# Kernel tuning notes

Hardware: AMD Instinct MI355X
Metric: run time of the kernel (lower is better)

## Reference

```python
import jax, jax.numpy as jnp
import numpy as np

N_NODES = 100000
K_NEIGH = 32
N_SAMPLE = 32
ITEM_LO, ITEM_HI = 0, 49999
EPS = 1e-12


def setup_inputs():
    key = jax.random.key(0)
    ks = jax.random.split(key, 16)
    B, T = 2048, 50
    D0, H, D2 = 64, 32, 64
    NU = 20000

    def nrm(k, shape, scale=0.05):
        return jax.random.normal(k, shape, dtype=jnp.float32) * scale

    return {
        "users": jax.random.randint(ks[0], (B,), 0, NU, dtype=jnp.int32),
        "pos": jax.random.randint(ks[1], (B,), 0, ITEM_HI + 1, dtype=jnp.int32),
        "neg": jax.random.randint(ks[2], (B,), 0, ITEM_HI + 1, dtype=jnp.int32),
        "train_set": jax.random.randint(ks[3], (B, T), 0, ITEM_HI + 1, dtype=jnp.int32),
        "adj_matrix": jax.random.randint(ks[4], (N_NODES, K_NEIGH), 0, N_NODES, dtype=jnp.int32),
        "edge_matrix": jax.random.randint(ks[5], (N_NODES, K_NEIGH), 0, N_NODES, dtype=jnp.int32),
        "entity_embedding": nrm(ks[6], (N_NODES, D0)),
        "Wl1": nrm(ks[7], (H, D0), 0.1),
        "bl1": jnp.zeros((H,), jnp.float32),
        "Wr1": nrm(ks[8], (H, D0), 0.1),
        "Wl2": nrm(ks[9], (D2, H), 0.1),
        "bl2": jnp.zeros((D2,), jnp.float32),
        "Wr2": nrm(ks[10], (D2, H), 0.1),
        "dis_user": nrm(ks[11], (NU, D2)),
        "dis_item": nrm(ks[12], (N_NODES, D2)),
    }


def _dropout(x, k, p=0.5):
    keep = jax.random.bernoulli(k, 1.0 - p, x.shape)
    return jnp.where(keep, x / (1.0 - p), 0.0)


def reference(users, pos, neg, train_set, adj_matrix, edge_matrix,
              entity_embedding, Wl1, bl1, Wr1, Wl2, bl2, Wr2,
              dis_user, dis_item):
    B = users.shape[0]
    # edge list: src = node_index repeated, dst = its sampled neighbors (build_edge)
    src = jnp.repeat(jnp.arange(N_NODES, dtype=jnp.int32), K_NEIGH)
    dst = edge_matrix.reshape(-1)
    cnt = jax.ops.segment_sum(jnp.ones_like(dst, jnp.float32), dst, num_segments=N_NODES)
    inv_cnt = (1.0 / jnp.maximum(cnt, 1.0))[:, None]

    def sage(x, Wl, bl, Wr):
        # PyG SAGEConv: lin_l(mean of messages at dst) + lin_r(x)
        agg = jax.ops.segment_sum(x[src], dst, num_segments=N_NODES) * inv_cnt
        return agg @ Wl.T + bl + x @ Wr.T

    def gcn(call_id):
        k = jax.random.fold_in(jax.random.key(42), call_id)
        k1, k2 = jax.random.split(k)
        h = _dropout(jax.nn.leaky_relu(sage(entity_embedding, Wl1, bl1, Wr1), 0.01), k1)
        h = _dropout(sage(h, Wl2, bl2, Wr2), k2)
        return h / jnp.maximum(jnp.linalg.norm(h, axis=1, keepdims=True), EPS)

    def kg_step(pos_ids, call_id, step):
        g = gcn(call_id)
        u_e = g[users]                    # [B,d]
        pos_e = g[pos_ids]                # [B,d]
        one_hop = adj_matrix[pos_ids]     # [B,K]
        i_e = g[one_hop]                  # [B,K,d]
        p = jnp.einsum('bkd,bd->bk', i_e, pos_e * u_e)
        logp = jax.nn.log_softmax(p, axis=1)
        if step == 1:
            nid = jnp.argmax(p, axis=1)[:, None]
        else:
            # torch.sort is ascending -> first num_sample are the LOWEST logits (as in source)
            nid = jnp.argsort(p, axis=1)[:, :N_SAMPLE]
        cand = jnp.take_along_axis(one_hop, nid, axis=1)
        clog = jnp.take_along_axis(logp, nid, axis=1)
        if step == 1:
            return cand[:, 0], clog[:, 0]
        return cand, clog

    def filter_entity(cand, k):
        rnd = jax.random.randint(k, cand.shape, ITEM_LO, ITEM_HI + 1, dtype=cand.dtype)
        bad = (cand < ITEM_LO) | (cand > ITEM_HI)
        return jnp.where(bad, rnd, cand)

    def dis_step(cand, clog):
        ranking = jnp.einsum('bd,bnd->bn', dis_user[users], dis_item[cand])
        idx = jnp.argmax(ranking, axis=1)[:, None]
        return (jnp.take_along_axis(cand, idx, axis=1)[:, 0],
                jnp.take_along_axis(clog, idx, axis=1)[:, 0])

    def filter_trainset(gneg):
        in_tr = jnp.any(gneg[:, None] == train_set, axis=1)
        return jnp.where(in_tr, neg, gneg)

    def one_round(pos_ids, base):
        oh, l1 = kg_step(pos_ids, base, 1)
        cand, l2 = kg_step(oh, base + 1, 2)
        cand = filter_entity(cand, jax.random.fold_in(jax.random.key(7), base))
        gneg, lsel = dis_step(cand, l2)
        gneg = filter_trainset(gneg)
        return gneg, l1 + lsel

    g1, lg1 = one_round(pos, 0)
    g2, lg2 = one_round(g1, 2)
    good_neg = jnp.stack([g1, g2], axis=1)        # [B, k_step]
    good_logits = jnp.stack([lg1, lg2], axis=1)   # [B, k_step]
    return good_neg, good_logits
```

## Files before the change

kernel.cpp:

```cpp
#include <hip/hip_runtime.h>
#include <hip/hip_bf16.h>
#include <stdint.h>

#define NND 100000
#define KN 32
#define NE (NND*KN)
#define BB 2048
#define TT 50
#define DD0 64
#define HH 32
#define DD2 64
#define NROWS 34
#define BSH 9
#define NBUK ((NND + (1<<BSH) - 1) >> BSH)
#define PCHUNK 6250

typedef unsigned long long ull;

__device__ __forceinline__ void tf2x32(uint32_t k0, uint32_t k1, uint32_t& x0, uint32_t& x1){
  uint32_t k2 = k0 ^ k1 ^ 0x1BD11BDAu;
#define TFR(r) { x0 += x1; x1 = (x1<<(r)) | (x1>>(32-(r))); x1 ^= x0; }
  x0 += k0; x1 += k1;
  TFR(13) TFR(15) TFR(26) TFR(6)
  x0 += k1; x1 += k2 + 1u;
  TFR(17) TFR(29) TFR(16) TFR(24)
  x0 += k2; x1 += k0 + 2u;
  TFR(13) TFR(15) TFR(26) TFR(6)
  x0 += k0; x1 += k1 + 3u;
  TFR(17) TFR(29) TFR(16) TFR(24)
  x0 += k1; x1 += k2 + 4u;
  TFR(13) TFR(15) TFR(26) TFR(6)
  x0 += k2; x1 += k0 + 5u;
#undef TFR
}

__device__ __forceinline__ uint32_t xorbits(uint32_t ka, uint32_t kb, uint32_t i){
  uint32_t x0=0u, x1=i;
  tf2x32(ka,kb,x0,x1);
  return x0^x1;
}

__global__ void keys_kernel(uint32_t* keys, int* bcnt){
  int t=threadIdx.x;
  for(int i=t;i<NBUK+1;i+=64) bcnt[i]=0;
  if(t==0 && blockIdx.x==0){
    for(int cid=0;cid<4;++cid){
      uint32_t K0=0u,K1=(uint32_t)cid;
      tf2x32(0u,42u,K0,K1);
      uint32_t a0=0u,a1=0u; tf2x32(K0,K1,a0,a1);
      uint32_t b0=0u,b1=1u; tf2x32(K0,K1,b0,b1);
      keys[cid*4+0]=a0; keys[cid*4+1]=a1;
      keys[cid*4+2]=b0; keys[cid*4+3]=b1;
    }
    for(int r=0;r<2;++r){
      uint32_t F0=0u,F1=(uint32_t)(2*r);
      tf2x32(0u,7u,F0,F1);
      uint32_t a0=0u,a1=0u; tf2x32(F0,F1,a0,a1);
      uint32_t b0=0u,b1=1u; tf2x32(F0,F1,b0,b1);
      keys[16+r*4+0]=a0; keys[16+r*4+1]=a1;
      keys[16+r*4+2]=b0; keys[16+r*4+3]=b1;
    }
  }
}

__global__ void __launch_bounds__(256) bcount_kernel(const int* __restrict__ edge, int* bcnt){
  __shared__ int h[NBUK];
  int t=threadIdx.x;
  for(int i=t;i<NBUK;i+=256) h[i]=0;
  __syncthreads();
  int start=blockIdx.x*PCHUNK, end=start+PCHUNK;
  for(int e=start+t;e<end;e+=256) atomicAdd(&h[edge[e]>>BSH],1);
  __syncthreads();
  for(int i=t;i<NBUK;i+=256) if(h[i]) atomicAdd(&bcnt[i],h[i]);
}

__global__ void bscan_kernel(const int* bcnt, int* boff, int* bcur, int* off){
  if(threadIdx.x==0 && blockIdx.x==0){
    int run=0;
    for(int i=0;i<NBUK;++i){ boff[i]=run; bcur[i]=run; run+=bcnt[i]; }
    boff[NBUK]=run;
    off[NND]=NE;
  }
}

__global__ void __launch_bounds__(256) bscatter_kernel(const int* __restrict__ edge,
    int* bcur, ull* __restrict__ tmp8){
  __shared__ int h[NBUK], base[NBUK], lcur[NBUK];
  int t=threadIdx.x;
  for(int i=t;i<NBUK;i+=256){ h[i]=0; lcur[i]=0; }
  __syncthreads();
  int start=blockIdx.x*PCHUNK, end=start+PCHUNK;
  for(int e=start+t;e<end;e+=256) atomicAdd(&h[edge[e]>>BSH],1);
  __syncthreads();
  for(int i=t;i<NBUK;i+=256) base[i] = h[i]? atomicAdd(&bcur[i],h[i]) : 0;
  __syncthreads();
  for(int e=start+t;e<end;e+=256){
    int d=edge[e];
    int b=d>>BSH;
    int r=atomicAdd(&lcur[b],1);
    tmp8[base[b]+r] = (((ull)(unsigned)d)<<32) | (unsigned)e;
  }
}

__global__ void __launch_bounds__(256) bucket_csr_kernel(const int* __restrict__ boff,
    const ull* __restrict__ tmp8, int* __restrict__ off, float* __restrict__ inv,
    int* __restrict__ col){
  __shared__ int cnt[512], pref[512], cur2[512];
  int b=blockIdx.x, t=threadIdx.x;
  int nb=b<<BSH;
  for(int i=t;i<512;i+=256) cnt[i]=0;
  __syncthreads();
  int lo=boff[b], hi=boff[b+1];
  for(int i=lo+t;i<hi;i+=256){
    int ld=(int)(tmp8[i]>>32)-nb;
    atomicAdd(&cnt[ld],1);
  }
  __syncthreads();
  if(t==0){ int run=lo; for(int i=0;i<512;++i){ pref[i]=run; cur2[i]=run; run+=cnt[i]; } }
  __syncthreads();
  for(int i=t;i<512;i+=256){
    int d=nb+i;
    if(d<NND){ off[d]=pref[i]; int c=cnt[i]; inv[d]=1.0f/(float)(c>0?c:1); }
  }
  __syncthreads();
  for(int i=lo+t;i<hi;i+=256){
    ull v=tmp8[i];
    int ld=(int)(v>>32)-nb;
    int r=atomicAdd(&cur2[ld],1);
    col[r]=(int)(v&0xffffffffu);
  }
}

__global__ void count_kernel(const int* dst, int* cnt){
  int e = blockIdx.x*256 + threadIdx.x;
  if(e < NE) atomicAdd(&cnt[dst[e]], 1);
}
__global__ void scan_kernel(const int* cnt, int* off, int* cur, float* inv){
  __shared__ int part[1024];
  int t = threadIdx.x;
  const int CH = (NND + 1023)/1024;
  int lo = t*CH, hi = lo+CH; if(hi>NND) hi=NND;
  int s=0;
  for(int i=lo;i<hi;++i) s += cnt[i];
  part[t]=s;
  __syncthreads();
  if(t==0){ int run=0; for(int i=0;i<1024;++i){ int v=part[i]; part[i]=run; run+=v; } }
  __syncthreads();
  int run = part[t];
  for(int i=lo;i<hi;++i){
    off[i]=run; cur[i]=run;
    int c=cnt[i];
    inv[i]=1.0f/(float)(c>0?c:1);
    run+=c;
  }
  if(t==0) off[NND]=NE;
}
__global__ void fill_kernel(const int* dst, int* cur, int* col){
  int e = blockIdx.x*256 + threadIdx.x;
  if(e < NE){
    int d = dst[e];
    int slot = atomicAdd(&cur[d],1);
    col[slot] = e;
  }
}

__global__ void __launch_bounds__(256) sortseg_wave_kernel(const int* off, int* col){
  int t=threadIdx.x, lane=t&63, w=t>>6;
  int node = blockIdx.x*4 + w;
  if(node>=NND) return;
  int lo=off[node], hi=off[node+1];
  int deg=hi-lo;
  if(deg<=1) return;
  if(deg<=64){
    int v = (lane<deg)? col[lo+lane] : 0x7fffffff;
    for(int p=0;p<64;++p){
      int partner;
      if((p&1)==0) partner = lane^1;
      else partner = (lane==0||lane==63)? lane : ((lane&1)? lane+1 : lane-1);
      int pv = __shfl(v, partner, 64);
      if(partner>lane) v = v<pv? v:pv;
      else if(partner<lane) v = v>pv? v:pv;
    }
    if(lane<deg) col[lo+lane]=v;
  } else if(lane==0){
    for(int i=lo+1;i<hi;++i){
      int v=col[i]; int j=i-1;
      while(j>=lo && col[j]>v){ col[j+1]=col[j]; --j; }
      col[j+1]=v;
    }
  }
}

__device__ __forceinline__ float gather_seq(const float* __restrict__ src, int S, int d,
    const int* __restrict__ col, int lo, int hi, int lane){
  float acc=0.f;
  int deg=hi-lo, base=0;
  while(base<deg){
    int rem=deg-base; int cw = rem<64?rem:64;
    int cv = col[lo+base+ (lane<cw?lane:cw-1)];
    for(int k=0;k<cw;k+=16){
      int m=cw-k;
      float v[16];
#pragma unroll
      for(int j=0;j<16;++j){
        int q = (j<m)? k+j : k;
        int s = __shfl(cv,q,64)>>5;
        v[j] = src[(size_t)s*S+d];
      }
#pragma unroll
      for(int j=0;j<16;++j) if(j<m) acc += v[j];
    }
    base+=cw;
  }
  return acc;
}

__device__ __forceinline__ float gather_seq32(const float* __restrict__ src, int S, int d,
    const int* __restrict__ col, int lo, int hi, int l){
  float acc=0.f;
  int deg=hi-lo, base=0;
  while(base<deg){
    int rem=deg-base; int cw = rem<32?rem:32;
    int cv = col[lo+base+ (l<cw?l:cw-1)];
    for(int k=0;k<cw;k+=16){
      int m=cw-k;
      float v[16];
#pragma unroll
      for(int j=0;j<16;++j){
        int q = (j<m)? k+j : k;
        int s = __shfl(cv,q,32)>>5;
        v[j] = src[(size_t)s*S+d];
      }
#pragma unroll
      for(int j=0;j<16;++j) if(j<m) acc += v[j];
    }
    base+=cw;
  }
  return acc;
}

__global__ void __launch_bounds__(512) sage1base_kernel(const float* __restrict__ x,
    const int* __restrict__ off, const int* __restrict__ col,
    const float* __restrict__ inv, const float* __restrict__ Wl,
    const float* __restrict__ bl, const float* __restrict__ Wr,
    float* __restrict__ h1base){
  __shared__ float sWlT[DD0*HH], sWrT[DD0*HH];
  __shared__ float sA[8][DD0], sX[8][DD0];
  int t=threadIdx.x, lane=t&63, w=t>>6;
  for(int j=t;j<HH*DD0;j+=512){
    int k=j>>5, h=j&31;
    sWlT[j]=Wl[h*DD0+k]; sWrT[j]=Wr[h*DD0+k];
  }
  int node=blockIdx.x*8+w;
  int lo=off[node], hi=off[node+1];
  float acc=gather_seq(x,DD0,lane,col,lo,hi,lane);
  acc *= inv[node];
  sA[w][lane]=acc;
  sX[w][lane]=x[(size_t)node*DD0+lane];
  __syncthreads();
  if(lane<HH){
    float s1=0.f, s2=0.f;
    for(int k=0;k<DD0;++k){
      s1 += sA[w][k]*sWlT[k*HH+lane];
      s2 += sX[w][k]*sWrT[k*HH+lane];
    }
    float v=s1+bl[lane]+s2;
    v = (v>=0.f) ? v : 0.01f*v;
    h1base[(size_t)node*HH+lane]=v;
  }
}

__global__ void __launch_bounds__(256) mask_kernel(const float* __restrict__ h1base,
    const uint32_t* __restrict__ keys, int cid, float* __restrict__ h1){
  int j = blockIdx.x*256 + threadIdx.x;
  if(j < NND*HH){
    uint32_t bits = xorbits(keys[cid*4+0],keys[cid*4+1],(uint32_t)j);
    float v = h1base[j];
    h1[j] = ((bits>>31)==0u) ? 2.f*v : 0.f;
  }
}

__global__ void __launch_bounds__(256) sage1_kernel(const float* __restrict__ x,
    const int* __restrict__ off, const int* __restrict__ col,
    const float* __restrict__ inv, const float* __restrict__ Wl,
    const float* __restrict__ bl, const float* __restrict__ Wr,
    const uint32_t* __restrict__ keys, int cid, float* __restrict__ h1o){
  __shared__ float sWlT[DD0*HH], sWrT[DD0*HH];
  __shared__ float sA[4][DD0], sX[4][DD0];
  int t=threadIdx.x, lane=t&63, w=t>>6;
  for(int j=t;j<HH*DD0;j+=256){
    int k=j>>5, h=j&31;
    sWlT[j]=Wl[h*DD0+k]; sWrT[j]=Wr[h*DD0+k];
  }
  int node=blockIdx.x*4+w;
  int lo=off[node], hi=off[node+1];
  float acc=gather_seq(x,DD0,lane,col,lo,hi,lane);
  acc *= inv[node];
  sA[w][lane]=acc;
  sX[w][lane]=x[(size_t)node*DD0+lane];
  __syncthreads();
  if(lane<HH){
    float s1=0.f, s2=0.f;
    for(int k=0;k<DD0;++k){
      s1 += sA[w][k]*sWlT[k*HH+lane];
      s2 += sX[w][k]*sWrT[k*HH+lane];
    }
    float v=s1+bl[lane]+s2;
    v = (v>=0.f) ? v : 0.01f*v;
    uint32_t j=(uint32_t)(node*HH+lane);
    uint32_t bits = xorbits(keys[cid*4+0],keys[cid*4+1],j);
    v = ((bits>>31)==0u) ? 2.f*v : 0.f;
    h1o[(size_t)node*HH+lane]=v;
  }
}

__device__ __forceinline__ float g_row_core(int n, int lane,
    const float* __restrict__ h1, const int* __restrict__ off,
    const int* __restrict__ col, const float* __restrict__ inv,
    const float* __restrict__ sWlT, const float* __restrict__ sWrT,
    const float* __restrict__ bl2, uint32_t k2a, uint32_t k2b){
  int lo=off[n], hi=off[n+1];
  int d=lane&31;
  float acc=gather_seq(h1,HH,d,col,lo,hi,lane);
  float aggd = acc*inv[n];
  float hd   = h1[(size_t)n*HH+d];
  float s1=0.f, s2=0.f;
  for(int k=0;k<HH;++k){
    float ak=__shfl(aggd,k,64);
    float hk=__shfl(hd,k,64);
    s1 += ak*sWlT[k*DD2+lane];
    s2 += hk*sWrT[k*DD2+lane];
  }
  float v=s1+bl2[lane]+s2;
  uint32_t j=(uint32_t)n*64u+(uint32_t)lane;
  uint32_t bits = xorbits(k2a,k2b,j);
  v = ((bits>>31)==0u) ? 2.f*v : 0.f;
  float ss=v*v;
  for(int m=1;m<64;m<<=1) ss += __shfl_xor(ss,m,64);
  return v/fmaxf(sqrtf(ss),1e-12f);
}

__global__ void __launch_bounds__(512) grows2_kernel(
    const float* __restrict__ h1, const int* __restrict__ off,
    const int* __restrict__ col, const float* __restrict__ inv,
    const float* __restrict__ Wl2, const float* __restrict__ bl2,
    const float* __restrict__ Wr2, const uint32_t* __restrict__ keys, int cid,
    const int* __restrict__ users, const int* __restrict__ pid_arr,
    const int* __restrict__ adj, float* __restrict__ rowbuf){
  __shared__ float sWlT[HH*DD2], sWrT[HH*DD2];
  int t=threadIdx.x, lane=t&63, w=t>>6;
  int half=lane>>5, l=lane&31;
  for(int j=t;j<HH*DD2;j+=512){
    int k=j>>6, d=j&63;
    sWlT[j]=Wl2[d*HH+k]; sWrT[j]=Wr2[d*HH+k];
  }
  __syncthreads();
  int wg = blockIdx.x*16 + w*2 + half;
  int b = wg/NROWS, r = wg - b*NROWS;
  int pid = pid_arr[b];
  int node = (r==0)? users[b] : ((r==1)? pid : adj[(size_t)pid*KN + (r-2)]);
  uint32_t k2a=keys[cid*4+2], k2b=keys[cid*4+3];
  int lo=off[node], hi=off[node+1];
  float acc = gather_seq32(h1,HH,l,col,lo,hi,l);
  float aggd = acc*inv[node];
  float hd   = h1[(size_t)node*HH+l];
  float s1a=0.f,s2a=0.f,s1b=0.f,s2b=0.f;
  for(int k=0;k<HH;++k){
    float ak=__shfl(aggd,k,32);
    float hk=__shfl(hd,k,32);
    s1a += ak*sWlT[k*DD2+l];      s2a += hk*sWrT[k*DD2+l];
    s1b += ak*sWlT[k*DD2+l+32];   s2b += hk*sWrT[k*DD2+l+32];
  }
  float va=s1a+bl2[l]+s2a;
  float vb=s1b+bl2[l+32]+s2b;
  uint32_t ja=(uint32_t)node*64u+(uint32_t)l;
  va = ((xorbits(k2a,k2b,ja)>>31)==0u)     ? 2.f*va : 0.f;
  vb = ((xorbits(k2a,k2b,ja+32u)>>31)==0u) ? 2.f*vb : 0.f;
  float ssa=va*va, ssb=vb*vb;
  for(int m=1;m<32;m<<=1){ ssa += __shfl_xor(ssa,m,32); ssb += __shfl_xor(ssb,m,32); }
  float nr=fmaxf(sqrtf(ssa+ssb),1e-12f);
  rowbuf[(size_t)wg*DD2 + l]      = va/nr;
  rowbuf[(size_t)wg*DD2 + l + 32] = vb/nr;
}

__global__ void __launch_bounds__(64) sel1_kernel(
    const float* __restrict__ rowbuf,
    const int* __restrict__ users, const int* __restrict__ pid_arr,
    const int* __restrict__ adj, int* __restrict__ oh_out, float* __restrict__ l1_out){
  int b=blockIdx.x, t=threadIdx.x;
  __shared__ float wsh[DD2];
  __shared__ float ps[KN];
  const float* rb = rowbuf + (size_t)b*NROWS*DD2;
  wsh[t] = rb[t]*rb[DD2+t];
  __syncthreads();
  if(t<KN){
    float p=0.f;
    const float* rr = rb + (size_t)(2+t)*DD2;
    for(int d=0;d<DD2;++d) p += rr[d]*wsh[d];
    ps[t]=p;
  }
  __syncthreads();
  if(t==0){
    float m=ps[0]; for(int k=1;k<KN;++k) m=fmaxf(m,ps[k]);
    float s=0.f;  for(int k=0;k<KN;++k) s += expf(ps[k]-m);
    int best=0; float bv=ps[0];
    for(int k=1;k<KN;++k) if(ps[k]>bv){bv=ps[k];best=k;}
    oh_out[b]=adj[(size_t)pid_arr[b]*KN+best];
    l1_out[b]=(ps[best]-m)-logf(s);
  }
}

__global__ void __launch_bounds__(64) sel2_kernel(
    const float* __restrict__ rowbuf, const uint32_t* __restrict__ keys, int kf_idx,
    const int* __restrict__ users, const int* __restrict__ oh,
    const int* __restrict__ adj,
    const float* __restrict__ du, const float* __restrict__ di,
    const int* __restrict__ train, const int* __restrict__ neg,
    const float* __restrict__ l1, int round,
    int* __restrict__ gneg_out, float* __restrict__ out){
  int b=blockIdx.x, t=threadIdx.x;
  __shared__ float wsh[DD2];
  __shared__ float ps[KN], lps[KN], rk[KN];
  __shared__ int nid[KN], cand[KN];
  __shared__ float msh[2];
  const float* rb = rowbuf + (size_t)b*NROWS*DD2;
  wsh[t] = rb[t]*rb[DD2+t];
  __syncthreads();
  if(t<KN){
    float p=0.f;
    const float* rr = rb + (size_t)(2+t)*DD2;
    for(int d=0;d<DD2;++d) p += rr[d]*wsh[d];
    ps[t]=p;
  }
  __syncthreads();
  if(t==0){
    float m=ps[0]; for(int k=1;k<KN;++k) m=fmaxf(m,ps[k]);
    float s=0.f;  for(int k=0;k<KN;++k) s += expf(ps[k]-m);
    msh[0]=m; msh[1]=logf(s);
    for(int k=0;k<KN;++k) nid[k]=k;
    for(int i=1;i<KN;++i){
      int v=nid[i]; float pv=ps[v]; int j=i-1;
      while(j>=0 && ps[nid[j]]>pv){ nid[j+1]=nid[j]; --j; }
      nid[j+1]=v;
    }
  }
  __syncthreads();
  if(t<KN){
    int n=t, c=adj[(size_t)oh[b]*KN + nid[n]];
    if(c<0 || c>49999){
      uint32_t i0=(uint32_t)(b*KN+n);
      const uint32_t* fk = keys + 16 + kf_idx*4;
      uint32_t hb = xorbits(fk[0], fk[1], i0);
      uint32_t lb = xorbits(fk[2], fk[3], i0);
      c=(int)(((hb%50000u)*17296u + (lb%50000u))%50000u);
    }
    cand[n]=c;
    lps[n]=(ps[nid[n]]-msh[0])-msh[1];
    int u=users[b];
    float rr=0.f;
    for(int d=0;d<DD2;++d) rr += du[(size_t)u*DD2+d]*di[(size_t)c*DD2+d];
    rk[n]=rr;
  }
  __syncthreads();
  if(t==0){
    int best=0; float bv=rk[0];
    for(int n=1;n<KN;++n) if(rk[n]>bv){bv=rk[n];best=n;}
    int gn=cand[best]; float lsel=lps[best];
    bool it=false;
    for(int t2=0;t2<TT;++t2) if(train[(size_t)b*TT+t2]==gn){it=true;break;}
    if(it) gn=neg[b];
    gneg_out[b]=gn;
    out[b*2+round]        = (float)gn;
    out[BB*2 + b*2+round] = l1[b]+lsel;
  }
}

__global__ void __launch_bounds__(256) fstep1_kernel(
    const float* __restrict__ h1, const int* __restrict__ off,
    const int* __restrict__ col, const float* __restrict__ inv,
    const float* __restrict__ Wl2, const float* __restrict__ bl2,
    const float* __restrict__ Wr2, const uint32_t* __restrict__ keys, int cid,
    const int* __restrict__ users, const int* __restrict__ pid_arr,
    const int* __restrict__ adj, int* __restrict__ oh_out, float* __restrict__ l1_out){
  __shared__ float sWlT[HH*DD2], sWrT[HH*DD2];
  __shared__ float rows[2+KN][DD2+1];
  __shared__ int nds[2+KN];
  __shared__ float ps[KN];
  int t=threadIdx.x, lane=t&63, w=t>>6, b=blockIdx.x;
  for(int j=t;j<HH*DD2;j+=256){
    int k=j>>6, d=j&63;
    sWlT[j]=Wl2[d*HH+k]; sWrT[j]=Wr2[d*HH+k];
  }
  if(t==0){ nds[0]=users[b]; nds[1]=pid_arr[b]; }
  if(t>=2 && t<2+KN) nds[t]=adj[(size_t)pid_arr[b]*KN + (t-2)];
  __syncthreads();
  uint32_t k2a=keys[cid*4+2], k2b=keys[cid*4+3];
  for(int r=w; r<2+KN; r+=4)
    rows[r][lane]=g_row_core(nds[r],lane,h1,off,col,inv,sWlT,sWrT,bl2,k2a,k2b);
  __syncthreads();
  if(t<KN){
    float p=0.f;
    for(int d=0;d<DD2;++d) p += rows[2+t][d]*(rows[0][d]*rows[1][d]);
    ps[t]=p;
  }
  __syncthreads();
  if(t==0){
    float m=ps[0]; for(int k=1;k<KN;++k) m=fmaxf(m,ps[k]);
    float s=0.f;  for(int k=0;k<KN;++k) s += expf(ps[k]-m);
    int best=0; float bv=ps[0];
    for(int k=1;k<KN;++k) if(ps[k]>bv){bv=ps[k];best=k;}
    oh_out[b]=nds[2+best];
    l1_out[b]=(ps[best]-m)-logf(s);
  }
}

__global__ void __launch_bounds__(256) fstep2_kernel(
    const float* __restrict__ h1, const int* __restrict__ off,
    const int* __restrict__ col, const float* __restrict__ inv,
    const float* __restrict__ Wl2, const float* __restrict__ bl2,
    const float* __restrict__ Wr2, const uint32_t* __restrict__ keys,
    int cid, int kf_idx,
    const int* __restrict__ users, const int* __restrict__ oh,
    const int* __restrict__ adj,
    const float* __restrict__ du, const float* __restrict__ di,
    const int* __restrict__ train, const int* __restrict__ neg,
    const float* __restrict__ l1, int round,
    int* __restrict__ gneg_out, float* __restrict__ out){
  __shared__ float sWlT[HH*DD2], sWrT[HH*DD2];
  __shared__ float rows[2+KN][DD2+1];
  __shared__ int nds[2+KN];
  __shared__ float ps[KN], lps[KN], rk[KN];
  __shared__ int nid[KN], cand[KN];
  __shared__ float msh[2];
  int t=threadIdx.x, lane=t&63, w=t>>6, b=blockIdx.x;
  for(int j=t;j<HH*DD2;j+=256){
    int k=j>>6, d=j&63;
    sWlT[j]=Wl2[d*HH+k]; sWrT[j]=Wr2[d*HH+k];
  }
  if(t==0){ nds[0]=users[b]; nds[1]=oh[b]; }
  if(t>=2 && t<2+KN) nds[t]=adj[(size_t)oh[b]*KN + (t-2)];
  __syncthreads();
  uint32_t k2a=keys[cid*4+2], k2b=keys[cid*4+3];
  for(int r=w; r<2+KN; r+=4)
    rows[r][lane]=g_row_core(nds[r],lane,h1,off,col,inv,sWlT,sWrT,bl2,k2a,k2b);
  __syncthreads();
  if(t<KN){
    float p=0.f;
    for(int d=0;d<DD2;++d) p += rows[2+t][d]*(rows[0][d]*rows[1][d]);
    ps[t]=p;
  }
  __syncthreads();
  if(t==0){
    float m=ps[0]; for(int k=1;k<KN;++k) m=fmaxf(m,ps[k]);
    float s=0.f;  for(int k=0;k<KN;++k) s += expf(ps[k]-m);
    msh[0]=m; msh[1]=logf(s);
    for(int k=0;k<KN;++k) nid[k]=k;
    for(int i=1;i<KN;++i){
      int v=nid[i]; float pv=ps[v]; int j=i-1;
      while(j>=0 && ps[nid[j]]>pv){ nid[j+1]=nid[j]; --j; }
      nid[j+1]=v;
    }
  }
  __syncthreads();
  if(t<KN){
    int n=t, c=nds[2+nid[n]];
    if(c<0 || c>49999){
      uint32_t i0=(uint32_t)(b*KN+n);
      const uint32_t* fk = keys + 16 + kf_idx*4;
      uint32_t hb = xorbits(fk[0], fk[1], i0);
      uint32_t lb = xorbits(fk[2], fk[3], i0);
      c=(int)(((hb%50000u)*17296u + (lb%50000u))%50000u);
    }
    cand[n]=c;
    lps[n]=(ps[nid[n]]-msh[0])-msh[1];
    int u=nds[0];
    float rr=0.f;
    for(int d=0;d<DD2;++d) rr += du[(size_t)u*DD2+d]*di[(size_t)c*DD2+d];
    rk[n]=rr;
  }
  __syncthreads();
  if(t==0){
    int best=0; float bv=rk[0];
    for(int n=1;n<KN;++n) if(rk[n]>bv){bv=rk[n];best=n;}
    int gn=cand[best]; float lsel=lps[best];
    bool it=false;
    for(int t2=0;t2<TT;++t2) if(train[(size_t)b*TT+t2]==gn){it=true;break;}
    if(it) gn=neg[b];
    gneg_out[b]=gn;
    out[b*2+round]        = (float)gn;
    out[BB*2 + b*2+round] = l1[b]+lsel;
  }
}

extern "C" void kernel_launch(void* const* d_in, const int* in_sizes, int n_in,
                              void* d_out, int out_size, void* d_ws, size_t ws_size,
                              hipStream_t stream) {
  const int*   users=(const int*)d_in[0];
  const int*   pos  =(const int*)d_in[1];
  const int*   neg  =(const int*)d_in[2];
  const int*   train=(const int*)d_in[3];
  const int*   adj  =(const int*)d_in[4];
  const int*   edge =(const int*)d_in[5];
  const float* ent  =(const float*)d_in[6];
  const float* Wl1  =(const float*)d_in[7];
  const float* bl1  =(const float*)d_in[8];
  const float* Wr1  =(const float*)d_in[9];
  const float* Wl2  =(const float*)d_in[10];
  const float* bl2  =(const float*)d_in[11];
  const float* Wr2  =(const float*)d_in[12];
  const float* du   =(const float*)d_in[13];
  const float* di   =(const float*)d_in[14];
  float* out=(float*)d_out;

  char* wsb=(char*)d_ws;
  size_t o=0;
  auto alloc=[&](size_t n)->char*{ char* p=wsb+o; o=(o+n+255)&~(size_t)255; return p; };
  uint32_t* keys=(uint32_t*)alloc(32*4);
  int*   bcnt=(int*)alloc((size_t)(NBUK+1)*4);
  int*   boff=(int*)alloc((size_t)(NBUK+1)*4);
  int*   bcur=(int*)alloc((size_t)NBUK*4);
  int*   ohb=(int*)alloc((size_t)BB*4);
  float* l1b=(float*)alloc((size_t)BB*4);
  int*   g1b=(int*)alloc((size_t)BB*4);
  int*   g2b=(int*)alloc((size_t)BB*4);
  int*   cnt=(int*)alloc((size_t)NND*4);
  int*   off=(int*)alloc((size_t)(NND+1)*4);
  int*   cur=(int*)alloc((size_t)NND*4);
  float* inv=(float*)alloc((size_t)NND*4);
  int*   col=(int*)alloc((size_t)NE*4);
  float* h1 =(float*)alloc((size_t)NND*HH*4);
  float* rowbuf=(float*)alloc((size_t)BB*NROWS*DD2*4);
  size_t o_rowbuf = o;
  float* h1base=(float*)alloc((size_t)NND*HH*4);
  int tier = (ws_size >= o) ? 2 : ((ws_size >= o_rowbuf) ? 1 : 0);
  ull* tmp8 = (ull*)rowbuf;

  keys_kernel<<<1,64,0,stream>>>(keys,bcnt);

  if(tier==2){
    bcount_kernel<<<512,256,0,stream>>>(edge,bcnt);
    bscan_kernel<<<1,64,0,stream>>>(bcnt,boff,bcur,off);
    bscatter_kernel<<<512,256,0,stream>>>(edge,bcur,tmp8);
    bucket_csr_kernel<<<NBUK,256,0,stream>>>(boff,tmp8,off,inv,col);
  } else {
    hipMemsetAsync(cnt,0,(size_t)NND*4,stream);
    count_kernel<<<NE/256,256,0,stream>>>(edge,cnt);
    scan_kernel<<<1,1024,0,stream>>>(cnt,off,cur,inv);
    fill_kernel<<<NE/256,256,0,stream>>>(edge,cur,col);
  }
  sortseg_wave_kernel<<<NND/4,256,0,stream>>>(off,col);

  const int GROWS2_GRID = BB*NROWS/16;
  const int MASK_GRID   = (NND*HH+255)/256;

  if(tier==2){
    sage1base_kernel<<<NND/8,512,0,stream>>>(ent,off,col,inv,Wl1,bl1,Wr1,h1base);
    for(int r=0;r<2;++r){
      const int* pid = (r==0)? pos : g1b;
      int cidA=2*r, cidB=2*r+1;
      mask_kernel<<<MASK_GRID,256,0,stream>>>(h1base,keys,cidA,h1);
      grows2_kernel<<<GROWS2_GRID,512,0,stream>>>(h1,off,col,inv,Wl2,bl2,Wr2,keys,cidA,
                                                  users,pid,adj,rowbuf);
      sel1_kernel<<<BB,64,0,stream>>>(rowbuf,users,pid,adj,ohb,l1b);
      mask_kernel<<<MASK_GRID,256,0,stream>>>(h1base,keys,cidB,h1);
      grows2_kernel<<<GROWS2_GRID,512,0,stream>>>(h1,off,col,inv,Wl2,bl2,Wr2,keys,cidB,
                                                  users,ohb,adj,rowbuf);
      sel2_kernel<<<BB,64,0,stream>>>(rowbuf,keys,r,users,ohb,adj,du,di,train,neg,l1b,r,
                                      (r==0)?g1b:g2b,out);
    }
  } else if(tier==1){
    for(int r=0;r<2;++r){
      const int* pid = (r==0)? pos : g1b;
      int cidA=2*r, cidB=2*r+1;
      sage1_kernel<<<NND/4,256,0,stream>>>(ent,off,col,inv,Wl1,bl1,Wr1,keys,cidA,h1);
      grows2_kernel<<<GROWS2_GRID,512,0,stream>>>(h1,off,col,inv,Wl2,bl2,Wr2,keys,cidA,
                                                  users,pid,adj,rowbuf);
      sel1_kernel<<<BB,64,0,stream>>>(rowbuf,users,pid,adj,ohb,l1b);
      sage1_kernel<<<NND/4,256,0,stream>>>(ent,off,col,inv,Wl1,bl1,Wr1,keys,cidB,h1);
      grows2_kernel<<<GROWS2_GRID,512,0,stream>>>(h1,off,col,inv,Wl2,bl2,Wr2,keys,cidB,
                                                  users,ohb,adj,rowbuf);
      sel2_kernel<<<BB,64,0,stream>>>(rowbuf,keys,r,users,ohb,adj,du,di,train,neg,l1b,r,
                                      (r==0)?g1b:g2b,out);
    }
  } else {
    for(int r=0;r<2;++r){
      const int* pid = (r==0)? pos : g1b;
      int cidA=2*r, cidB=2*r+1;
      sage1_kernel<<<NND/4,256,0,stream>>>(ent,off,col,inv,Wl1,bl1,Wr1,keys,cidA,h1);
      fstep1_kernel<<<BB,256,0,stream>>>(h1,off,col,inv,Wl2,bl2,Wr2,keys,cidA,
                                         users,pid,adj,ohb,l1b);
      sage1_kernel<<<NND/4,256,0,stream>>>(ent,off,col,inv,Wl1,bl1,Wr1,keys,cidB,h1);
      fstep2_kernel<<<BB,256,0,stream>>>(h1,off,col,inv,Wl2,bl2,Wr2,keys,cidB,r,
                                         users,ohb,adj,du,di,train,neg,l1b,r,
                                         (r==0)?g1b:g2b,out);
    }
  }
}
```

Before: 855.4 us.

## Deduplicate layer-2 SAGE row computations via node flags and a per-node table

Adds a new top tier. A mark kernel flags every node needed by the selection step. A grid over all nodes then computes the layer-2 SAGE output once per flagged node into a node-indexed table, replacing one computation per (batch, row) slot. The selection kernels now read from that table by node id. The CSR column array is also shifted once after sorting, so the gather loops no longer shift each neighbour index. In exchange it adds a memset, mark launches and a larger workspace, and it launches blocks over all nodes, many of which only load the weights and exit.

```diff
diff --git a/kernel.cpp b/kernel.cpp
--- a/kernel.cpp
+++ b/kernel.cpp
@@ -191,6 +191,11 @@
   }
 }
 
+__global__ void srcify_kernel(int* col){
+  int i = blockIdx.x*256 + threadIdx.x;
+  if(i < NE) col[i] >>= 5;
+}
+
 __device__ __forceinline__ float gather_seq(const float* __restrict__ src, int S, int d,
     const int* __restrict__ col, int lo, int hi, int lane){
   float acc=0.f;
@@ -204,7 +209,7 @@
 #pragma unroll
       for(int j=0;j<16;++j){
         int q = (j<m)? k+j : k;
-        int s = __shfl(cv,q,64)>>5;
+        int s = __shfl(cv,q,64);
         v[j] = src[(size_t)s*S+d];
       }
 #pragma unroll
@@ -228,7 +233,7 @@
 #pragma unroll
       for(int j=0;j<16;++j){
         int q = (j<m)? k+j : k;
-        int s = __shfl(cv,q,32)>>5;
+        int s = __shfl(cv,q,32);
         v[j] = src[(size_t)s*S+d];
       }
 #pragma unroll
@@ -340,6 +345,34 @@
   return v/fmaxf(sqrtf(ss),1e-12f);
 }
 
+__device__ __forceinline__ void g_row_half(int node, int l,
+    const float* __restrict__ h1, const int* __restrict__ off,
+    const int* __restrict__ col, const float* __restrict__ inv,
+    const float* __restrict__ sWlT, const float* __restrict__ sWrT,
+    const float* __restrict__ bl2, uint32_t k2a, uint32_t k2b,
+    float* oa, float* ob){
+  int lo=off[node], hi=off[node+1];
+  float acc = gather_seq32(h1,HH,l,col,lo,hi,l);
+  float aggd = acc*inv[node];
+  float hd   = h1[(size_t)node*HH+l];
+  float s1a=0.f,s2a=0.f,s1b=0.f,s2b=0.f;
+  for(int k=0;k<HH;++k){
+    float ak=__shfl(aggd,k,32);
+    float hk=__shfl(hd,k,32);
+    s1a += ak*sWlT[k*DD2+l];      s2a += hk*sWrT[k*DD2+l];
+    s1b += ak*sWlT[k*DD2+l+32];   s2b += hk*sWrT[k*DD2+l+32];
+  }
+  float va=s1a+bl2[l]+s2a;
+  float vb=s1b+bl2[l+32]+s2b;
+  uint32_t ja=(uint32_t)node*64u+(uint32_t)l;
+  va = ((xorbits(k2a,k2b,ja)>>31)==0u)     ? 2.f*va : 0.f;
+  vb = ((xorbits(k2a,k2b,ja+32u)>>31)==0u) ? 2.f*vb : 0.f;
+  float ssa=va*va, ssb=vb*vb;
+  for(int m=1;m<32;m<<=1){ ssa += __shfl_xor(ssa,m,32); ssb += __shfl_xor(ssb,m,32); }
+  float nr=fmaxf(sqrtf(ssa+ssb),1e-12f);
+  *oa = va/nr; *ob = vb/nr;
+}
+
 __global__ void __launch_bounds__(512) grows2_kernel(
     const float* __restrict__ h1, const int* __restrict__ off,
     const int* __restrict__ col, const float* __restrict__ inv,
@@ -359,28 +392,137 @@
   int b = wg/NROWS, r = wg - b*NROWS;
   int pid = pid_arr[b];
   int node = (r==0)? users[b] : ((r==1)? pid : adj[(size_t)pid*KN + (r-2)]);
-  uint32_t k2a=keys[cid*4+2], k2b=keys[cid*4+3];
-  int lo=off[node], hi=off[node+1];
-  float acc = gather_seq32(h1,HH,l,col,lo,hi,l);
-  float aggd = acc*inv[node];
-  float hd   = h1[(size_t)node*HH+l];
-  float s1a=0.f,s2a=0.f,s1b=0.f,s2b=0.f;
-  for(int k=0;k<HH;++k){
-    float ak=__shfl(aggd,k,32);
-    float hk=__shfl(hd,k,32);
-    s1a += ak*sWlT[k*DD2+l];      s2a += hk*sWrT[k*DD2+l];
-    s1b += ak*sWlT[k*DD2+l+32];   s2b += hk*sWrT[k*DD2+l+32];
-  }
-  float va=s1a+bl2[l]+s2a;
-  float vb=s1b+bl2[l+32]+s2b;
-  uint32_t ja=(uint32_t)node*64u+(uint32_t)l;
-  va = ((xorbits(k2a,k2b,ja)>>31)==0u)     ? 2.f*va : 0.f;
-  vb = ((xorbits(k2a,k2b,ja+32u)>>31)==0u) ? 2.f*vb : 0.f;
-  float ssa=va*va, ssb=vb*vb;
-  for(int m=1;m<32;m<<=1){ ssa += __shfl_xor(ssa,m,32); ssb += __shfl_xor(ssb,m,32); }
-  float nr=fmaxf(sqrtf(ssa+ssb),1e-12f);
-  rowbuf[(size_t)wg*DD2 + l]      = va/nr;
-  rowbuf[(size_t)wg*DD2 + l + 32] = vb/nr;
+  float va,vb;
+  g_row_half(node,l,h1,off,col,inv,sWlT,sWrT,bl2,keys[cid*4+2],keys[cid*4+3],&va,&vb);
+  rowbuf[(size_t)wg*DD2 + l]      = va;
+  rowbuf[(size_t)wg*DD2 + l + 32] = vb;
+}
+
+__global__ void __launch_bounds__(256) mark_kernel(const int* __restrict__ users,
+    const int* __restrict__ pid_arr, const int* __restrict__ adj,
+    int* __restrict__ flags, int gen){
+  int i = blockIdx.x*256 + threadIdx.x;
+  if(i >= BB*NROWS) return;
+  int b = i/NROWS, r = i - b*NROWS;
+  int pid = pid_arr[b];
+  int node = (r==0)? users[b] : ((r==1)? pid : adj[(size_t)pid*KN + (r-2)]);
+  flags[node] = gen;
+}
+
+__global__ void __launch_bounds__(512) grows_dedup_kernel(
+    const float* __restrict__ h1, const int* __restrict__ off,
+    const int* __restrict__ col, const float* __restrict__ inv,
+    const float* __restrict__ Wl2, const float* __restrict__ bl2,
+    const float* __restrict__ Wr2, const uint32_t* __restrict__ keys, int cid,
+    const int* __restrict__ flags, int gen, float* __restrict__ gtab){
+  __shared__ float sWlT[HH*DD2], sWrT[HH*DD2];
+  int t=threadIdx.x, lane=t&63, w=t>>6;
+  int half=lane>>5, l=lane&31;
+  for(int j=t;j<HH*DD2;j+=512){
+    int k=j>>6, d=j&63;
+    sWlT[j]=Wl2[d*HH+k]; sWrT[j]=Wr2[d*HH+k];
+  }
+  __syncthreads();
+  int node = blockIdx.x*16 + w*2 + half;
+  if(node >= NND) return;
+  if(flags[node] != gen) return;
+  float va,vb;
+  g_row_half(node,l,h1,off,col,inv,sWlT,sWrT,bl2,keys[cid*4+2],keys[cid*4+3],&va,&vb);
+  gtab[(size_t)node*DD2 + l]      = va;
+  gtab[(size_t)node*DD2 + l + 32] = vb;
+}
+
+__global__ void __launch_bounds__(64) sel1d_kernel(
+    const float* __restrict__ gtab,
+    const int* __restrict__ users, const int* __restrict__ pid_arr,
+    const int* __restrict__ adj, int* __restrict__ oh_out, float* __restrict__ l1_out){
+  int b=blockIdx.x, t=threadIdx.x;
+  __shared__ float wsh[DD2];
+  __shared__ float ps[KN];
+  int u=users[b], pid=pid_arr[b];
+  wsh[t] = gtab[(size_t)u*DD2+t]*gtab[(size_t)pid*DD2+t];
+  __syncthreads();
+  if(t<KN){
+    int nb2=adj[(size_t)pid*KN+t];
+    float p=0.f;
+    const float* rr = gtab + (size_t)nb2*DD2;
+    for(int d=0;d<DD2;++d) p += rr[d]*wsh[d];
+    ps[t]=p;
+  }
+  __syncthreads();
+  if(t==0){
+    float m=ps[0]; for(int k=1;k<KN;++k) m=fmaxf(m,ps[k]);
+    float s=0.f;  for(int k=0;k<KN;++k) s += expf(ps[k]-m);
+    int best=0; float bv=ps[0];
+    for(int k=1;k<KN;++k) if(ps[k]>bv){bv=ps[k];best=k;}
+    oh_out[b]=adj[(size_t)pid*KN+best];
+    l1_out[b]=(ps[best]-m)-logf(s);
+  }
+}
+
+__global__ void __launch_bounds__(64) sel2d_kernel(
+    const float* __restrict__ gtab, const uint32_t* __restrict__ keys, int kf_idx,
+    const int* __restrict__ users, const int* __restrict__ oh,
+    const int* __restrict__ adj,
+    const float* __restrict__ du, const float* __restrict__ di,
+    const int* __restrict__ train, const int* __restrict__ neg,
+    const float* __restrict__ l1, int round,
+    int* __restrict__ gneg_out, float* __restrict__ out){
+  int b=blockIdx.x, t=threadIdx.x;
+  __shared__ float wsh[DD2];
+  __shared__ float ps[KN], lps[KN], rk[KN];
+  __shared__ int nid[KN], cand[KN];
+  __shared__ float msh[2];
+  int u=users[b], pid=oh[b];
+  wsh[t] = gtab[(size_t)u*DD2+t]*gtab[(size_t)pid*DD2+t];
+  __syncthreads();
+  if(t<KN){
+    int nb2=adj[(size_t)pid*KN+t];
+    float p=0.f;
+    const float* rr = gtab + (size_t)nb2*DD2;
+    for(int d=0;d<DD2;++d) p += rr[d]*wsh[d];
+    ps[t]=p;
+  }
+  __syncthreads();
+  if(t==0){
+    float m=ps[0]; for(int k=1;k<KN;++k) m=fmaxf(m,ps[k]);
+    float s=0.f;  for(int k=0;k<KN;++k) s += expf(ps[k]-m);
+    msh[0]=m; msh[1]=logf(s);
+    for(int k=0;k<KN;++k) nid[k]=k;
+    for(int i=1;i<KN;++i){
+      int v=nid[i]; float pv=ps[v]; int j=i-1;
+      while(j>=0 && ps[nid[j]]>pv){ nid[j+1]=nid[j]; --j; }
+      nid[j+1]=v;
+    }
+  }
+  __syncthreads();
+  if(t<KN){
+    int n=t, c=adj[(size_t)pid*KN + nid[n]];
+    if(c<0 || c>49999){
+      uint32_t i0=(uint32_t)(b*KN+n);
+      const uint32_t* fk = keys + 16 + kf_idx*4;
+      uint32_t hb = xorbits(fk[0], fk[1], i0);
+      uint32_t lb = xorbits(fk[2], fk[3], i0);
+      c=(int)(((hb%50000u)*17296u + (lb%50000u))%50000u);
+    }
+    cand[n]=c;
+    lps[n]=(ps[nid[n]]-msh[0])-msh[1];
+    float rr=0.f;
+    for(int d=0;d<DD2;++d) rr += du[(size_t)u*DD2+d]*di[(size_t)c*DD2+d];
+    rk[n]=rr;
+  }
+  __syncthreads();
+  if(t==0){
+    int best=0; float bv=rk[0];
+    for(int n=1;n<KN;++n) if(rk[n]>bv){bv=rk[n];best=n;}
+    int gn=cand[best]; float lsel=lps[best];
+    bool it=false;
+    for(int t2=0;t2<TT;++t2) if(train[(size_t)b*TT+t2]==gn){it=true;break;}
+    if(it) gn=neg[b];
+    gneg_out[b]=gn;
+    out[b*2+round]        = (float)gn;
+    out[BB*2 + b*2+round] = l1[b]+lsel;
+  }
 }
 
 __global__ void __launch_bounds__(64) sel1_kernel(
@@ -632,12 +774,16 @@
   float* rowbuf=(float*)alloc((size_t)BB*NROWS*DD2*4);
   size_t o_rowbuf = o;
   float* h1base=(float*)alloc((size_t)NND*HH*4);
-  int tier = (ws_size >= o) ? 2 : ((ws_size >= o_rowbuf) ? 1 : 0);
+  size_t o_tier2 = o;
+  int*   flags=(int*)alloc((size_t)NND*4);
+  float* gtab =(float*)alloc((size_t)NND*DD2*4);
+  size_t o_tier3 = o;
+  int tier = (ws_size >= o_tier3) ? 3 : ((ws_size >= o_tier2) ? 2 : ((ws_size >= o_rowbuf) ? 1 : 0));
   ull* tmp8 = (ull*)rowbuf;
 
   keys_kernel<<<1,64,0,stream>>>(keys,bcnt);
 
-  if(tier==2){
+  if(tier>=2){
     bcount_kernel<<<512,256,0,stream>>>(edge,bcnt);
     bscan_kernel<<<1,64,0,stream>>>(bcnt,boff,bcur,off);
     bscatter_kernel<<<512,256,0,stream>>>(edge,bcur,tmp8);
@@ -649,11 +795,35 @@
     fill_kernel<<<NE/256,256,0,stream>>>(edge,cur,col);
   }
   sortseg_wave_kernel<<<NND/4,256,0,stream>>>(off,col);
+  srcify_kernel<<<NE/256,256,0,stream>>>(col);
 
   const int GROWS2_GRID = BB*NROWS/16;
+  const int GDEDUP_GRID = (NND+15)/16;
+  const int MARK_GRID   = (BB*NROWS+255)/256;
   const int MASK_GRID   = (NND*HH+255)/256;
 
-  if(tier==2){
+  if(tier==3){
+    hipMemsetAsync(flags,0,(size_t)NND*4,stream);
+    sage1base_kernel<<<NND/8,512,0,stream>>>(ent,off,col,inv,Wl1,bl1,Wr1,h1base);
+    int gen=0;
+    for(int r=0;r<2;++r){
+      const int* pid = (r==0)? pos : g1b;
+      int cidA=2*r, cidB=2*r+1;
+      ++gen;
+      mask_kernel<<<MASK_GRID,256,0,stream>>>(h1base,keys,cidA,h1);
+      mark_kernel<<<MARK_GRID,256,0,stream>>>(users,pid,adj,flags,gen);
+      grows_dedup_kernel<<<GDEDUP_GRID,512,0,stream>>>(h1,off,col,inv,Wl2,bl2,Wr2,keys,cidA,
+                                                       flags,gen,gtab);
+      sel1d_kernel<<<BB,64,0,stream>>>(gtab,users,pid,adj,ohb,l1b);
+      ++gen;
+      mask_kernel<<<MASK_GRID,256,0,stream>>>(h1base,keys,cidB,h1);
+      mark_kernel<<<MARK_GRID,256,0,stream>>>(users,ohb,adj,flags,gen);
+      grows_dedup_kernel<<<GDEDUP_GRID,512,0,stream>>>(h1,off,col,inv,Wl2,bl2,Wr2,keys,cidB,
+                                                       flags,gen,gtab);
+      sel2d_kernel<<<BB,64,0,stream>>>(gtab,keys,r,users,ohb,adj,du,di,train,neg,l1b,r,
+                                       (r==0)?g1b:g2b,out);
+    }
+  } else if(tier==2){
     sage1base_kernel<<<NND/8,512,0,stream>>>(ent,off,col,inv,Wl1,bl1,Wr1,h1base);
     for(int r=0;r<2;++r){
       const int* pid = (r==0)? pos : g1b;
```

Result: slower. 926.0 us (+8.3%).
